# Optimization experiments

Measured on AMD Instinct MI355X. Metric: run time of the kernel, lower is better.

Reference implementation:

```python
import jax, jax.numpy as jnp
import numpy as np

H = 64   # hidden_layers
D = 1    # frame_dimension
N = 2048 # n_samples (batch)
T = 512  # seq_len


def setup_inputs() -> dict:
    key = jax.random.key(0)
    ks = jax.random.split(key, 12)
    s = 1.0 / np.sqrt(H)
    u = lambda k, shape: jax.random.uniform(k, shape, jnp.float32, -s, s)
    return {
        "y": jax.random.normal(ks[0], (N, T), dtype=jnp.float32),
        "W_ih1": u(ks[1], (4 * H, D)),
        "W_hh1": u(ks[2], (4 * H, H)),
        "b_ih1": u(ks[3], (4 * H,)),
        "b_hh1": u(ks[4], (4 * H,)),
        "W_ih2": u(ks[5], (4 * H, H)),
        "W_hh2": u(ks[6], (4 * H, H)),
        "b_ih2": u(ks[7], (4 * H,)),
        "b_hh2": u(ks[8], (4 * H,)),
        "W_lin": u(ks[9], (D, H)),
        "b_lin": u(ks[10], (D,)),
        "pre_output_len": 1,
    }


def _lstm_cell(x, h, c, W_ih, W_hh, b_ih, b_hh):
    # gates in PyTorch LSTMCell order: input, forget, cell(g), output
    g = x @ W_ih.T + b_ih + h @ W_hh.T + b_hh  # [n, 4H]
    i, f, gg, o = jnp.split(g, 4, axis=-1)
    i = jax.nn.sigmoid(i)
    f = jax.nn.sigmoid(f)
    gg = jnp.tanh(gg)
    o = jax.nn.sigmoid(o)
    c2 = f * c + i * gg
    h2 = o * jnp.tanh(c2)
    return h2, c2


def reference(y, W_ih1, W_hh1, b_ih1, b_hh1, W_ih2, W_hh2, b_ih2, b_hh2,
              W_lin, b_lin, pre_output_len):
    n = y.shape[0]
    zeros = jnp.zeros((n, H), dtype=jnp.float32)
    init = (zeros, zeros, zeros, zeros)

    def step(carry, x_t):
        h1, c1, h2, c2 = carry
        h1, c1 = _lstm_cell(x_t, h1, c1, W_ih1, W_hh1, b_ih1, b_hh1)
        h2, c2 = _lstm_cell(h1, h2, c2, W_ih2, W_hh2, b_ih2, b_hh2)
        out = h2 @ W_lin.T + b_lin  # [n, D]
        return (h1, c1, h2, c2), out

    ys = jnp.swapaxes(y, 0, 1)[:, :, None]  # [T, n, 1]
    _, outs = jax.lax.scan(step, init, ys)  # [T, n, D]
    outs = outs[pre_output_len:]            # drop first pre_output_len steps (static)
    # torch.cat along dim=1 of [n, D] chunks -> [n, (T - pre)*D]
    return jnp.transpose(outs, (1, 0, 2)).reshape(n, -1)
```

## Files before the change

kernel.cpp:

```cpp
#include <hip/hip_runtime.h>


typedef __attribute__((ext_vector_type(4))) int i32x4;
typedef __attribute__((ext_vector_type(4))) float f32x4;

#define XPITCH 2060
#define XP 0
#define HB 32960
#define HPL(layer, P, L) (HB + ((((layer) * 2 + (P)) * 2) + (L)) * 1280)
#define RING 43200
#define LDS_BYTES 75968
#define L2E 1.44269504f
#define N2L2E (-2.8853900817779268f)

__device__ __forceinline__ float fast_rcp(float x) { return __builtin_amdgcn_rcpf(x); }
__device__ __forceinline__ float exp2_f(float x) {
  float r; asm("v_exp_f32 %0, %1" : "=v"(r) : "v"(x)); return r;
}
__device__ __forceinline__ i32x4 mfma_i8(i32x4 a, i32x4 b, i32x4 c) {
  return __builtin_amdgcn_mfma_i32_16x16x64_i8(a, b, c, 0, 0, 0);
}
__device__ __forceinline__ void cell2(float i, float f, float g, float o,
                                      float& c, float& h) {
  const float ei = exp2_f(-i), ef = exp2_f(-f), eg = exp2_f(-g), eo = exp2_f(-o);
  const float P = (1.f - eg) * fast_rcp((1.f + ei) * (1.f + eg));
  c = fmaf(c, fast_rcp(1.f + ef), P);
  const float cc = fminf(15.f, fmaxf(-15.f, c));
  const float ec = exp2_f(N2L2E * cc);
  h = (1.f - ec) * fast_rcp((1.f + eo) * (1.f + ec));
}
__device__ __forceinline__ void quantW16(const float* p, i32x4& w0v, i32x4& w1v) {
  int b0[16], b1[16];
#pragma unroll
  for (int e = 0; e < 16; ++e) {
    const float v = p[e];
    const float q0 = rintf(v * 512.f);
    const float r = v - q0 * (1.f / 512.f);
    const float q1 = fminf(127.f, fmaxf(-127.f, rintf(r * 131072.f)));
    b0[e] = (int)q0;
    b1[e] = (int)q1;
  }
#pragma unroll
  for (int d = 0; d < 4; ++d) {
    w0v[d] = (b0[4 * d] & 255) | ((b0[4 * d + 1] & 255) << 8) |
             ((b0[4 * d + 2] & 255) << 16) | ((b0[4 * d + 3] & 255) << 24);
    w1v[d] = (b1[4 * d] & 255) | ((b1[4 * d + 1] & 255) << 8) |
             ((b1[4 * d + 2] & 255) << 16) | ((b1[4 * d + 3] & 255) << 24);
  }
}
__device__ __forceinline__ void quantH4(const float* h, unsigned& L0, unsigned& L1) {
  int q0[4], q1[4];
#pragma unroll
  for (int r = 0; r < 4; ++r) {
    const float q0f = rintf(h[r] * 64.f);
    q0[r] = (int)q0f;
    const float rr = h[r] - q0f * 0.015625f;
    const float q1f = fminf(127.f, fmaxf(-127.f, rintf(rr * 16384.f)));
    q1[r] = (int)q1f;
  }
  L0 = (q0[0] & 255) | ((q0[1] & 255) << 8) | ((q0[2] & 255) << 16) |
       ((q0[3] & 255) << 24);
  L1 = (q1[0] & 255) | ((q1[1] & 255) << 8) | ((q1[2] & 255) << 16) |
       ((q1[3] & 255) << 24);
}

__global__ __launch_bounds__(512, 2) void lstm2_r15(
    const float* __restrict__ y, const float* __restrict__ Wih1,
    const float* __restrict__ Whh1, const float* __restrict__ bih1,
    const float* __restrict__ bhh1, const float* __restrict__ Wih2,
    const float* __restrict__ Whh2, const float* __restrict__ bih2,
    const float* __restrict__ bhh2, const float* __restrict__ Wlin,
    const float* __restrict__ blin, float* __restrict__ out) {
  extern __shared__ char smem[];
  const int tid = threadIdx.x;
  const int w = tid >> 6;
  const int lane = tid & 63;
  const int g = lane >> 4;
  const int s = lane & 15;
  const int s0 = blockIdx.x * 16;

  for (int i = tid; i < 16 * 512; i += 512) {
    const int ss = i >> 9, t = i & 511;
    *(float*)(smem + XP + ss * XPITCH + t * 4) = y[(size_t)(s0 + ss) * 512 + t];
  }
  for (int i = tid; i < 10240 / 4; i += 512) *(float*)(smem + HB + i * 4) = 0.f;
  const float bl0 = blin[0];
  __syncthreads();

  const int boff = s * 80 + 16 * g;
  const float gsc[4] = {L2E, L2E, 2.0f * L2E, L2E};
  const i32x4 zeroi = {0, 0, 0, 0};
  float sc00[4], scB[4];
#pragma unroll
  for (int p = 0; p < 4; ++p) {
    sc00[p] = gsc[p] * (1.f / 32768.f);
    scB[p] = gsc[p] * (1.f / 8388608.f);
  }

  if (w < 4) {
    const int row = 16 * w + s;
    i32x4 aW0[4], aW1[4];
#pragma unroll
    for (int p = 0; p < 4; ++p)
      quantW16(Whh1 + (size_t)(p * 64 + row) * 64 + 16 * g, aW0[p], aW1[p]);
    float bias1c[4][4], wih1c[4][4];
#pragma unroll
    for (int p = 0; p < 4; ++p)
#pragma unroll
      for (int r = 0; r < 4; ++r) {
        const int rr = p * 64 + 16 * w + 4 * g + r;
        bias1c[p][r] = (bih1[rr] + bhh1[rr]) * gsc[p];
        wih1c[p][r] = Wih1[rr] * gsc[p];
      }
    float c1[4] = {0.f, 0.f, 0.f, 0.f};
    const int hwA = s * 80 + 16 * w + 4 * g;
    const float* xrow = (const float*)(smem + XP + s * XPITCH);

#define EB(KK, P)                                                             \
  {                                                                           \
    const float x = xrow[KK];                                                 \
    const i32x4 B0 = *(const i32x4*)(smem + HPL(0, (P) ^ 1, 0) + boff);       \
    const i32x4 B1 = *(const i32x4*)(smem + HPL(0, (P) ^ 1, 1) + boff);       \
    i32x4 S00[4], SB[4];                                                      \
    __builtin_amdgcn_s_setprio(1);                                            \
    _Pragma("unroll") for (int p = 0; p < 4; ++p)                             \
        S00[p] = mfma_i8(aW0[p], B0, zeroi);                                  \
    _Pragma("unroll") for (int p = 0; p < 4; ++p)                             \
        SB[p] = mfma_i8(aW1[p], B0, zeroi);                                   \
    _Pragma("unroll") for (int p = 0; p < 4; ++p)                             \
        SB[p] = mfma_i8(aW0[p], B1, SB[p]);                                   \
    __builtin_amdgcn_s_setprio(0);                                            \
    float ga[4][4];                                                           \
    _Pragma("unroll") for (int p = 0; p < 4; ++p) {                           \
      _Pragma("unroll") for (int r = 0; r < 4; ++r) {                         \
        float base = fmaf(wih1c[p][r], x, bias1c[p][r]);                      \
        base = fmaf((float)SB[p][r], scB[p], base);                           \
        ga[p][r] = fmaf((float)S00[p][r], sc00[p], base);                     \
      }                                                                       \
    }                                                                         \
    float h1n[4];                                                             \
    _Pragma("unroll") for (int r = 0; r < 4; ++r)                             \
        cell2(ga[0][r], ga[1][r], ga[2][r], ga[3][r], c1[r], h1n[r]);         \
    unsigned L0, L1;                                                          \
    quantH4(h1n, L0, L1);                                                     \
    *(unsigned*)(smem + HPL(0, (P), 0) + hwA) = L0;                           \
    *(unsigned*)(smem + HPL(0, (P), 1) + hwA) = L1;                           \
  }

    EB(0, 0);
    __syncthreads();
#pragma unroll 1
    for (int kb = 1; kb <= 509; kb += 2) {
      EB(kb, 1);
      __syncthreads();
      EB(kb + 1, 0);
      __syncthreads();
    }
    EB(511, 1);
    __syncthreads();
    __syncthreads();
  } else {
    const int ow = w - 4;
    const int row = 16 * ow + s;
    i32x4 bW0[4], bW1[4], cW0[4], cW1[4];
#pragma unroll
    for (int p = 0; p < 4; ++p) {
      quantW16(Wih2 + (size_t)(p * 64 + row) * 64 + 16 * g, bW0[p], bW1[p]);
      quantW16(Whh2 + (size_t)(p * 64 + row) * 64 + 16 * g, cW0[p], cW1[p]);
    }
    float bias2c[4][4], wlinc[4];
#pragma unroll
    for (int p = 0; p < 4; ++p)
#pragma unroll
      for (int r = 0; r < 4; ++r) {
        const int rr = p * 64 + 16 * ow + 4 * g + r;
        bias2c[p][r] = (bih2[rr] + bhh2[rr]) * gsc[p];
      }
#pragma unroll
    for (int r = 0; r < 4; ++r) wlinc[r] = Wlin[16 * ow + 4 * g + r];
    float c2[4] = {0.f, 0.f, 0.f, 0.f};
    const int hwA = s * 80 + 16 * ow + 4 * g;
    char* ringb = smem + RING + ow * 64 + s * 4;

#define OFLUSH(KK)                                                            \
  if ((KK) >= 66 && (((KK)-2) & 63) == 0) {                                   \
    const int base = (KK)-66;                                                 \
    const int thr = ow * 64 + lane;                                           \
    const int ss2 = thr & 15, grp = thr >> 4;                                 \
    _Pragma("unroll") for (int q = 0; q < 4; ++q) {                           \
      const int idx = base + grp * 4 + q;                                     \
      const char* op = smem + RING + (idx & 127) * 256 + ss2 * 4;             \
      const float v = *(const float*)(op) + *(const float*)(op + 64) +        \
                      *(const float*)(op + 128) + *(const float*)(op + 192) + \
                      bl0;                                                    \
      out[(size_t)(s0 + ss2) * 511 + idx] = v;                                \
    }                                                                         \
  }

#define OB(KK, P)                                                             \
  {                                                                           \
    const i32x4 B10 = *(const i32x4*)(smem + HPL(0, (P) ^ 1, 0) + boff);      \
    const i32x4 B11 = *(const i32x4*)(smem + HPL(0, (P) ^ 1, 1) + boff);      \
    const i32x4 B20 = *(const i32x4*)(smem + HPL(1, (P), 0) + boff);          \
    const i32x4 B21 = *(const i32x4*)(smem + HPL(1, (P), 1) + boff);          \
    i32x4 S00[4], SB[4];                                                      \
    __builtin_amdgcn_s_setprio(1);                                            \
    _Pragma("unroll") for (int p = 0; p < 4; ++p)                             \
        S00[p] = mfma_i8(bW0[p], B10, zeroi);                                 \
    _Pragma("unroll") for (int p = 0; p < 4; ++p)                             \
        SB[p] = mfma_i8(bW1[p], B10, zeroi);                                  \
    _Pragma("unroll") for (int p = 0; p < 4; ++p)                             \
        S00[p] = mfma_i8(cW0[p], B20, S00[p]);                                \
    _Pragma("unroll") for (int p = 0; p < 4; ++p)                             \
        SB[p] = mfma_i8(bW0[p], B11, SB[p]);                                  \
    _Pragma("unroll") for (int p = 0; p < 4; ++p)                             \
        SB[p] = mfma_i8(cW1[p], B20, SB[p]);                                  \
    _Pragma("unroll") for (int p = 0; p < 4; ++p)                             \
        SB[p] = mfma_i8(cW0[p], B21, SB[p]);                                  \
    __builtin_amdgcn_s_setprio(0);                                            \
    float ga[4][4];                                                           \
    _Pragma("unroll") for (int p = 0; p < 4; ++p) {                           \
      _Pragma("unroll") for (int r = 0; r < 4; ++r) {                         \
        float base = fmaf((float)SB[p][r], scB[p], bias2c[p][r]);             \
        ga[p][r] = fmaf((float)S00[p][r], sc00[p], base);                     \
      }                                                                       \
    }                                                                         \
    float h2n[4];                                                             \
    _Pragma("unroll") for (int r = 0; r < 4; ++r)                             \
        cell2(ga[0][r], ga[1][r], ga[2][r], ga[3][r], c2[r], h2n[r]);         \
    unsigned L0, L1;                                                          \
    quantH4(h2n, L0, L1);                                                     \
    *(unsigned*)(smem + HPL(1, (P) ^ 1, 0) + hwA) = L0;                       \
    *(unsigned*)(smem + HPL(1, (P) ^ 1, 1) + hwA) = L1;                       \
    if ((KK) >= 2) {                                                          \
      float pw = wlinc[0] * h2n[0];                                           \
      pw = fmaf(wlinc[1], h2n[1], pw);                                        \
      pw = fmaf(wlinc[2], h2n[2], pw);                                        \
      pw = fmaf(wlinc[3], h2n[3], pw);                                        \
      pw += __shfl_xor(pw, 16, 64);                                           \
      pw += __shfl_xor(pw, 32, 64);                                           \
      if (g == 0) *(float*)(ringb + (((KK)-2) & 127) * 256) = pw;             \
    }                                                                         \
  }

    __syncthreads();
#pragma unroll 1
    for (int kb = 1; kb <= 509; kb += 2) {
      OB(kb, 1);
      __syncthreads();
      OFLUSH(kb + 1);
      OB(kb + 1, 0);
      __syncthreads();
    }
    OB(511, 1);
    __syncthreads();
    OB(512, 0);
    __syncthreads();
    {
      const int thr = ow * 64 + lane;
      for (int e = thr; e < 63 * 16; e += 256) {
        const int ss2 = e & 15, off = e >> 4;
        const int idx = 448 + off;
        const char* op = smem + RING + (idx & 127) * 256 + ss2 * 4;
        const float v = *(const float*)(op) + *(const float*)(op + 64) +
                        *(const float*)(op + 128) + *(const float*)(op + 192) + bl0;
        out[(size_t)(s0 + ss2) * 511 + idx] = v;
      }
    }
  }
}

extern "C" void kernel_launch(void* const* d_in, const int* in_sizes, int n_in,
                              void* d_out, int out_size, void* d_ws, size_t ws_size,
                              hipStream_t stream) {
  const float* y    = (const float*)d_in[0];
  const float* Wih1 = (const float*)d_in[1];
  const float* Whh1 = (const float*)d_in[2];
  const float* bih1 = (const float*)d_in[3];
  const float* bhh1 = (const float*)d_in[4];
  const float* Wih2 = (const float*)d_in[5];
  const float* Whh2 = (const float*)d_in[6];
  const float* bih2 = (const float*)d_in[7];
  const float* bhh2 = (const float*)d_in[8];
  const float* Wlin = (const float*)d_in[9];
  const float* blin = (const float*)d_in[10];
  float* out = (float*)d_out;

  hipFuncSetAttribute((const void*)lstm2_r15,
                      hipFuncAttributeMaxDynamicSharedMemorySize, LDS_BYTES);
  lstm2_r15<<<dim3(128), dim3(512), LDS_BYTES, stream>>>(
      y, Wih1, Whh1, bih1, bhh1, Wih2, Whh2, bih2, bhh2, Wlin, blin, out);
}
```

Baseline: 564.9 us.

## Pack two 16-sample groups per 1024-thread block and fold int8 partial sums

Each block now runs two independent 16-sample groups (64 blocks of 1024 threads instead of 128 of 512), each group with its own LDS slice for inputs, hidden-state buffers and output ring. The block-wide __syncthreads now couples both groups. The two int32 MFMA partial sums are combined as integers (S00<<8 + SB) before a single convert and FMA, and the negation is folded into the v_exp_f32 operand. Fewer blocks on a 256-CU device halves the CUs used, trading parallelism for wider blocks with larger LDS use.

```diff
diff --git a/kernel.cpp b/kernel.cpp
--- a/kernel.cpp
+++ b/kernel.cpp
@@ -5,11 +5,11 @@
 typedef __attribute__((ext_vector_type(4))) float f32x4;
 
 #define XPITCH 2060
-#define XP 0
-#define HB 32960
-#define HPL(layer, P, L) (HB + ((((layer) * 2 + (P)) * 2) + (L)) * 1280)
-#define RING 43200
-#define LDS_BYTES 75968
+#define XPG 32960
+#define HB0 65920
+#define HBG 10240
+#define RING0 86400
+#define LDS_BYTES 151936
 #define L2E 1.44269504f
 #define N2L2E (-2.8853900817779268f)
 
@@ -17,12 +17,15 @@
 __device__ __forceinline__ float exp2_f(float x) {
   float r; asm("v_exp_f32 %0, %1" : "=v"(r) : "v"(x)); return r;
 }
+__device__ __forceinline__ float exp2_nf(float x) {
+  float r; asm("v_exp_f32 %0, -%1" : "=v"(r) : "v"(x)); return r;
+}
 __device__ __forceinline__ i32x4 mfma_i8(i32x4 a, i32x4 b, i32x4 c) {
   return __builtin_amdgcn_mfma_i32_16x16x64_i8(a, b, c, 0, 0, 0);
 }
 __device__ __forceinline__ void cell2(float i, float f, float g, float o,
                                       float& c, float& h) {
-  const float ei = exp2_f(-i), ef = exp2_f(-f), eg = exp2_f(-g), eo = exp2_f(-o);
+  const float ei = exp2_nf(i), ef = exp2_nf(f), eg = exp2_nf(g), eo = exp2_nf(o);
   const float P = (1.f - eg) * fast_rcp((1.f + ei) * (1.f + eg));
   c = fmaf(c, fast_rcp(1.f + ef), P);
   const float cc = fminf(15.f, fmaxf(-15.f, c));
@@ -64,7 +67,7 @@
        ((q1[3] & 255) << 24);
 }
 
-__global__ __launch_bounds__(512, 2) void lstm2_r15(
+__global__ __launch_bounds__(1024, 4) void lstm2_r16(
     const float* __restrict__ y, const float* __restrict__ Wih1,
     const float* __restrict__ Whh1, const float* __restrict__ bih1,
     const float* __restrict__ bhh1, const float* __restrict__ Wih2,
@@ -74,31 +77,35 @@
   extern __shared__ char smem[];
   const int tid = threadIdx.x;
   const int w = tid >> 6;
+  const int q = w >> 3;
+  const int wr = w & 7;
   const int lane = tid & 63;
   const int g = lane >> 4;
   const int s = lane & 15;
-  const int s0 = blockIdx.x * 16;
-
-  for (int i = tid; i < 16 * 512; i += 512) {
+  const int s0g = blockIdx.x * 32 + q * 16;
+
+  for (int i = tid; i < 32 * 512; i += 1024) {
     const int ss = i >> 9, t = i & 511;
-    *(float*)(smem + XP + ss * XPITCH + t * 4) = y[(size_t)(s0 + ss) * 512 + t];
-  }
-  for (int i = tid; i < 10240 / 4; i += 512) *(float*)(smem + HB + i * 4) = 0.f;
+    *(float*)(smem + (ss >> 4) * XPG + (ss & 15) * XPITCH + t * 4) =
+        y[(size_t)(blockIdx.x * 32 + ss) * 512 + t];
+  }
+  for (int i = tid; i < 20480 / 4; i += 1024) *(float*)(smem + HB0 + i * 4) = 0.f;
   const float bl0 = blin[0];
   __syncthreads();
 
+  const int hq = HB0 + q * HBG;
+  const int ringB = RING0 + q * 32768;
   const int boff = s * 80 + 16 * g;
   const float gsc[4] = {L2E, L2E, 2.0f * L2E, L2E};
   const i32x4 zeroi = {0, 0, 0, 0};
-  float sc00[4], scB[4];
-#pragma unroll
-  for (int p = 0; p < 4; ++p) {
-    sc00[p] = gsc[p] * (1.f / 32768.f);
-    scB[p] = gsc[p] * (1.f / 8388608.f);
-  }
-
-  if (w < 4) {
-    const int row = 16 * w + s;
+  float scB[4];
+#pragma unroll
+  for (int p = 0; p < 4; ++p) scB[p] = gsc[p] * (1.f / 8388608.f);
+
+#define PL(layer, P, L) (hq + ((((layer) * 2 + (P)) * 2) + (L)) * 1280)
+
+  if (wr < 4) {
+    const int row = 16 * wr + s;
     i32x4 aW0[4], aW1[4];
 #pragma unroll
     for (int p = 0; p < 4; ++p)
@@ -108,19 +115,19 @@
     for (int p = 0; p < 4; ++p)
 #pragma unroll
       for (int r = 0; r < 4; ++r) {
-        const int rr = p * 64 + 16 * w + 4 * g + r;
+        const int rr = p * 64 + 16 * wr + 4 * g + r;
         bias1c[p][r] = (bih1[rr] + bhh1[rr]) * gsc[p];
         wih1c[p][r] = Wih1[rr] * gsc[p];
       }
     float c1[4] = {0.f, 0.f, 0.f, 0.f};
-    const int hwA = s * 80 + 16 * w + 4 * g;
-    const float* xrow = (const float*)(smem + XP + s * XPITCH);
+    const int hwA = s * 80 + 16 * wr + 4 * g;
+    const float* xrow = (const float*)(smem + q * XPG + s * XPITCH);
 
 #define EB(KK, P)                                                             \
   {                                                                           \
     const float x = xrow[KK];                                                 \
-    const i32x4 B0 = *(const i32x4*)(smem + HPL(0, (P) ^ 1, 0) + boff);       \
-    const i32x4 B1 = *(const i32x4*)(smem + HPL(0, (P) ^ 1, 1) + boff);       \
+    const i32x4 B0 = *(const i32x4*)(smem + PL(0, (P) ^ 1, 0) + boff);        \
+    const i32x4 B1 = *(const i32x4*)(smem + PL(0, (P) ^ 1, 1) + boff);        \
     i32x4 S00[4], SB[4];                                                      \
     __builtin_amdgcn_s_setprio(1);                                            \
     _Pragma("unroll") for (int p = 0; p < 4; ++p)                             \
@@ -133,9 +140,9 @@
     float ga[4][4];                                                           \
     _Pragma("unroll") for (int p = 0; p < 4; ++p) {                           \
       _Pragma("unroll") for (int r = 0; r < 4; ++r) {                         \
-        float base = fmaf(wih1c[p][r], x, bias1c[p][r]);                      \
-        base = fmaf((float)SB[p][r], scB[p], base);                           \
-        ga[p][r] = fmaf((float)S00[p][r], sc00[p], base);                     \
+        const int gi = (S00[p][r] << 8) + SB[p][r];                           \
+        const float base = fmaf(wih1c[p][r], x, bias1c[p][r]);                \
+        ga[p][r] = fmaf((float)gi, scB[p], base);                             \
       }                                                                       \
     }                                                                         \
     float h1n[4];                                                             \
@@ -143,8 +150,8 @@
         cell2(ga[0][r], ga[1][r], ga[2][r], ga[3][r], c1[r], h1n[r]);         \
     unsigned L0, L1;                                                          \
     quantH4(h1n, L0, L1);                                                     \
-    *(unsigned*)(smem + HPL(0, (P), 0) + hwA) = L0;                           \
-    *(unsigned*)(smem + HPL(0, (P), 1) + hwA) = L1;                           \
+    *(unsigned*)(smem + PL(0, (P), 0) + hwA) = L0;                            \
+    *(unsigned*)(smem + PL(0, (P), 1) + hwA) = L1;                            \
   }
 
     EB(0, 0);
@@ -160,7 +167,7 @@
     __syncthreads();
     __syncthreads();
   } else {
-    const int ow = w - 4;
+    const int ow = wr - 4;
     const int row = 16 * ow + s;
     i32x4 bW0[4], bW1[4], cW0[4], cW1[4];
 #pragma unroll
@@ -180,29 +187,29 @@
     for (int r = 0; r < 4; ++r) wlinc[r] = Wlin[16 * ow + 4 * g + r];
     float c2[4] = {0.f, 0.f, 0.f, 0.f};
     const int hwA = s * 80 + 16 * ow + 4 * g;
-    char* ringb = smem + RING + ow * 64 + s * 4;
+    char* ringb = smem + ringB + ow * 64 + s * 4;
 
 #define OFLUSH(KK)                                                            \
   if ((KK) >= 66 && (((KK)-2) & 63) == 0) {                                   \
     const int base = (KK)-66;                                                 \
     const int thr = ow * 64 + lane;                                           \
     const int ss2 = thr & 15, grp = thr >> 4;                                 \
-    _Pragma("unroll") for (int q = 0; q < 4; ++q) {                           \
-      const int idx = base + grp * 4 + q;                                     \
-      const char* op = smem + RING + (idx & 127) * 256 + ss2 * 4;             \
+    _Pragma("unroll") for (int qq = 0; qq < 4; ++qq) {                        \
+      const int idx = base + grp * 4 + qq;                                    \
+      const char* op = smem + ringB + (idx & 127) * 256 + ss2 * 4;            \
       const float v = *(const float*)(op) + *(const float*)(op + 64) +        \
                       *(const float*)(op + 128) + *(const float*)(op + 192) + \
                       bl0;                                                    \
-      out[(size_t)(s0 + ss2) * 511 + idx] = v;                                \
+      out[(size_t)(s0g + ss2) * 511 + idx] = v;                               \
     }                                                                         \
   }
 
 #define OB(KK, P)                                                             \
   {                                                                           \
-    const i32x4 B10 = *(const i32x4*)(smem + HPL(0, (P) ^ 1, 0) + boff);      \
-    const i32x4 B11 = *(const i32x4*)(smem + HPL(0, (P) ^ 1, 1) + boff);      \
-    const i32x4 B20 = *(const i32x4*)(smem + HPL(1, (P), 0) + boff);          \
-    const i32x4 B21 = *(const i32x4*)(smem + HPL(1, (P), 1) + boff);          \
+    const i32x4 B10 = *(const i32x4*)(smem + PL(0, (P) ^ 1, 0) + boff);       \
+    const i32x4 B11 = *(const i32x4*)(smem + PL(0, (P) ^ 1, 1) + boff);       \
+    const i32x4 B20 = *(const i32x4*)(smem + PL(1, (P), 0) + boff);           \
+    const i32x4 B21 = *(const i32x4*)(smem + PL(1, (P), 1) + boff);           \
     i32x4 S00[4], SB[4];                                                      \
     __builtin_amdgcn_s_setprio(1);                                            \
     _Pragma("unroll") for (int p = 0; p < 4; ++p)                             \
@@ -221,8 +228,8 @@
     float ga[4][4];                                                           \
     _Pragma("unroll") for (int p = 0; p < 4; ++p) {                           \
       _Pragma("unroll") for (int r = 0; r < 4; ++r) {                         \
-        float base = fmaf((float)SB[p][r], scB[p], bias2c[p][r]);             \
-        ga[p][r] = fmaf((float)S00[p][r], sc00[p], base);                     \
+        const int gi = (S00[p][r] << 8) + SB[p][r];                           \
+        ga[p][r] = fmaf((float)gi, scB[p], bias2c[p][r]);                     \
       }                                                                       \
     }                                                                         \
     float h2n[4];                                                             \
@@ -230,8 +237,8 @@
         cell2(ga[0][r], ga[1][r], ga[2][r], ga[3][r], c2[r], h2n[r]);         \
     unsigned L0, L1;                                                          \
     quantH4(h2n, L0, L1);                                                     \
-    *(unsigned*)(smem + HPL(1, (P) ^ 1, 0) + hwA) = L0;                       \
-    *(unsigned*)(smem + HPL(1, (P) ^ 1, 1) + hwA) = L1;                       \
+    *(unsigned*)(smem + PL(1, (P) ^ 1, 0) + hwA) = L0;                        \
+    *(unsigned*)(smem + PL(1, (P) ^ 1, 1) + hwA) = L1;                        \
     if ((KK) >= 2) {                                                          \
       float pw = wlinc[0] * h2n[0];                                           \
       pw = fmaf(wlinc[1], h2n[1], pw);                                        \
@@ -261,10 +268,10 @@
       for (int e = thr; e < 63 * 16; e += 256) {
         const int ss2 = e & 15, off = e >> 4;
         const int idx = 448 + off;
-        const char* op = smem + RING + (idx & 127) * 256 + ss2 * 4;
+        const char* op = smem + ringB + (idx & 127) * 256 + ss2 * 4;
         const float v = *(const float*)(op) + *(const float*)(op + 64) +
                         *(const float*)(op + 128) + *(const float*)(op + 192) + bl0;
-        out[(size_t)(s0 + ss2) * 511 + idx] = v;
+        out[(size_t)(s0g + ss2) * 511 + idx] = v;
       }
     }
   }
@@ -286,8 +293,8 @@
   const float* blin = (const float*)d_in[10];
   float* out = (float*)d_out;
 
-  hipFuncSetAttribute((const void*)lstm2_r15,
+  hipFuncSetAttribute((const void*)lstm2_r16,
                       hipFuncAttributeMaxDynamicSharedMemorySize, LDS_BYTES);
-  lstm2_r15<<<dim3(128), dim3(512), LDS_BYTES, stream>>>(
+  lstm2_r16<<<dim3(64), dim3(1024), LDS_BYTES, stream>>>(
       y, Wih1, Whh1, bih1, bhh1, Wih2, Whh2, bih2, bhh2, Wlin, blin, out);
 }
```

Result: slower. 1.618 ms (+186.3%).
